# Kernel tuning notes

Hardware: AMD Instinct MI355X
Metric: run time of the kernel (lower is better)

The kernel has to match this reference:

```python
import jax, jax.numpy as jnp
import numpy as np

# --- SLAYER params (nmnistNet.yaml) ---
THETA = 10.0
TS = 1.0
TAU_REF = 1.0
SCALE_REF = 2.0
T_SAMPLE = 300
B = 8

def _alpha_kernel(tau, mult, t_sample, ts, eps=0.01):
    vals = []
    t = 0.0
    while t < t_sample:
        v = mult * t / tau * np.exp(1.0 - t / tau)
        if abs(v) < eps and t > tau:
            break
        vals.append(v)
        t += ts
    return np.asarray(vals, np.float32)

# refractory kernel: alpha kernel with mult = -scaleRef*theta (slayer._calculateRefKernel)
REF_KERNEL = _alpha_kernel(TAU_REF, -SCALE_REF * THETA, T_SAMPLE, TS)
NREF = REF_KERNEL.shape[0]  # 11 for these params; REF_KERNEL[0] == 0


def spike(u):
    """slayerCuda.getSpikes: per-neuron sequential threshold recurrence over time.
    u: [..., T] membrane potential. On spike at t, REF_KERNEL is accumulated
    into u[t:t+NREF]; spike amplitude is 1/Ts."""
    uT = jnp.moveaxis(u, -1, 0)  # [T, ...]
    refk = jnp.asarray(REF_KERNEL[1:]).reshape((NREF - 1,) + (1,) * (u.ndim - 1))
    buf0 = jnp.zeros((NREF - 1,) + uT.shape[1:], u.dtype)  # pending refractory

    def step(buf, u_t):
        u_mod = u_t + buf[0]
        ev = (u_mod >= THETA).astype(u.dtype)
        buf = jnp.concatenate([buf[1:], jnp.zeros_like(buf[:1])], axis=0) + ev[None] * refk
        return buf, ev / TS

    _, s = jax.lax.scan(step, buf0, uT)
    return jnp.moveaxis(s, 0, -1)


def conv2d_t(x, w, pad):
    """slayer.conv: Conv3d with kernel (k,k,1) == per-timestep 2D conv.
    x: [B,C,H,W,T], w: [O,I,kh,kw]."""
    b, c, h, wd, t = x.shape
    xb = jnp.moveaxis(x, -1, 1).reshape(b * t, c, h, wd)
    y = jax.lax.conv_general_dilated(xb, w, (1, 1), [(pad, pad), (pad, pad)],
                                     dimension_numbers=('NCHW', 'OIHW', 'NCHW'))
    o, ho, wo = y.shape[1], y.shape[2], y.shape[3]
    return jnp.moveaxis(y.reshape(b, t, o, ho, wo), 1, -1)


def sum_pool2(x):
    """slayer.pool(2): fixed-weight (1.1*theta) 2x2/stride-2 sum over H,W per channel."""
    y = jax.lax.reduce_window(x, 0.0, jax.lax.add, (1, 1, 2, 2, 1), (1, 1, 2, 2, 1), 'VALID')
    return 1.1 * THETA * y


def setup_inputs():
    key = jax.random.key(0)
    k0, k1, k2, k3, k4 = jax.random.split(key, 5)
    spikeInput = (jax.random.uniform(k0, (B, 2, 34, 34, T_SAMPLE)) < 0.1).astype(jnp.float32) / TS
    # conv weights: kaiming-uniform bound * 100 (the __init__ scales conv weights by 100)
    w1 = jax.random.uniform(k1, (16, 2, 5, 5), minval=-14.1, maxval=14.1, dtype=jnp.float32)
    w2 = jax.random.uniform(k2, (32, 16, 3, 3), minval=-8.3, maxval=8.3, dtype=jnp.float32)
    w3 = jax.random.uniform(k3, (64, 32, 3, 3), minval=-5.9, maxval=5.9, dtype=jnp.float32)
    wfc = jax.random.uniform(k4, (10, 64, 8, 8), minval=-0.5, maxval=0.5, dtype=jnp.float32)
    return {"spikeInput": spikeInput, "w1": w1, "w2": w2, "w3": w3, "wfc": wfc}


def reference(spikeInput, w1, w2, w3, wfc):
    s1 = spike(conv2d_t(spikeInput, w1, 1))  # [B,16,32,32,T]
    s2 = spike(sum_pool2(s1))                # [B,16,16,16,T]
    s3 = spike(conv2d_t(s2, w2, 1))          # [B,32,16,16,T]
    s4 = spike(sum_pool2(s3))                # [B,32,8,8,T]
    s5 = spike(conv2d_t(s4, w3, 1))          # [B,64,8,8,T]
    # dense((8,8,64),10): Conv3d(64,10,(8,8,1)) == full-spatial contraction
    u = jnp.einsum('bchwt,ochw->bot', s5, wfc)[:, :, None, None, :]
    return spike(u)                          # [B,10,1,1,T]
```

## Files before the change

### kernel.cpp

```cpp
#include <hip/hip_runtime.h>
#include <hip/hip_bf16.h>
#include <cmath>

#define T_SAMPLE 300
#define NCHUNK 75

typedef __attribute__((ext_vector_type(8))) short short8;
typedef __attribute__((ext_vector_type(4))) float f32x4;

struct RefK { float v[10]; };

__device__ __forceinline__ unsigned char spike_step(float u, float* buf, const RefK& rk) {
    const float um = u + buf[0];
    const bool fire = um >= 10.0f;
    const float ev = fire ? 1.0f : 0.0f;
#pragma unroll
    for (int r = 0; r < 9; ++r) buf[r] = fmaf(ev, rk.v[r], buf[r + 1]);
    buf[9] = ev * rk.v[9];
    return fire ? (unsigned char)1 : (unsigned char)0;
}

__device__ __forceinline__ short8 bytes_to_bf16x8(uint2 w8) {
    union { uint4 u; short8 s8; } cv;
    cv.u.x = (w8.x & 0xFFu) * 0x3F80u | ((((w8.x >> 8) & 0xFFu) * 0x3F80u) << 16);
    cv.u.y = ((w8.x >> 16) & 0xFFu) * 0x3F80u | ((((w8.x >> 24) & 0xFFu) * 0x3F80u) << 16);
    cv.u.z = (w8.y & 0xFFu) * 0x3F80u | ((((w8.y >> 8) & 0xFFu) * 0x3F80u) << 16);
    cv.u.w = ((w8.y >> 16) & 0xFFu) * 0x3F80u | ((((w8.y >> 24) & 0xFFu) * 0x3F80u) << 16);
    return cv.s8;
}

__device__ __forceinline__ unsigned short bf16_split_sel(float w, int s) {
    __hip_bfloat16 hb = __float2bfloat16(w);
    const float hf = __bfloat162float(hb);
    __hip_bfloat16 mb = __float2bfloat16(w - hf);
    const float mf = __bfloat162float(mb);
    __hip_bfloat16 lb = __float2bfloat16(w - hf - mf);
    __hip_bfloat16 sel = (s == 0) ? hb : ((s == 1) ? mb : lb);
    return *(unsigned short*)&sel;
}

__global__ __launch_bounds__(256) void transpose_in_k(
    const float* __restrict__ In, unsigned int* __restrict__ X)
{
    __shared__ unsigned int lds[16 * NCHUNK];
    const int blk = blockIdx.x;
    const int tn = threadIdx.x >> 4;
    const int tq = threadIdx.x & 15;
    const size_t n = (size_t)blk * 16 + tn;
#pragma unroll
    for (int p = 0; p < 5; ++p) {
        const int ch = p * 16 + tq;
        if (ch < NCHUNK) {
            const float4 v = *(const float4*)(In + n * T_SAMPLE + ch * 4);
            unsigned int u = (v.x != 0.f ? 1u : 0u) | (v.y != 0.f ? 0x100u : 0u) |
                             (v.z != 0.f ? 0x10000u : 0u) | (v.w != 0.f ? 0x1000000u : 0u);
            lds[tn * NCHUNK + ch] = u;
        }
    }
    __syncthreads();
    for (int idx = threadIdx.x; idx < 16 * NCHUNK; idx += 256) {
        const int ch = idx >> 4, t2 = idx & 15;
        X[(size_t)ch * 18496 + blk * 16 + t2] = lds[t2 * NCHUNK + ch];
    }
}

__global__ __launch_bounds__(256) void prep_w1_k(
    const float* __restrict__ w1, unsigned short* __restrict__ Wr1)
{
    const int g = blockIdx.x * 256 + threadIdx.x;
    const int j = g & 7;
    const int lane = (g >> 3) & 63;
    const int ks = (g >> 9) & 3;
    const int s = g >> 11;
    const int q = lane >> 4;
    const int oc = lane & 15;
    const int kg = ks * 32 + q * 8 + j;
    const int slot = kg >> 2, c = kg & 1;
    const int dy = slot / 6, dx = slot % 6;
    const float w = (dy < 5 && dx < 5) ? w1[((oc * 2 + c) * 5 + dy) * 5 + dx] * 0.5f : 0.f;
    Wr1[g] = bf16_split_sel(w, s);
}

__global__ __launch_bounds__(256) void prep_w3_k(
    const float* __restrict__ w3, unsigned short* __restrict__ Wr)
{
    const int g = blockIdx.x * 256 + threadIdx.x;
    const int j = g & 7;
    const int lane = (g >> 3) & 63;
    const int mt = (g >> 9) & 3;
    const int rest = g >> 11;
    const int ks = rest % 9;
    const int s = rest / 9;
    const int oc = mt * 16 + (lane & 15);
    const int ic = (lane >> 4) * 8 + j;
    Wr[g] = bf16_split_sel(w3[(oc * 32 + ic) * 9 + ks], s);
}

__global__ __launch_bounds__(256) void prep_w2_k(
    const float* __restrict__ w2, unsigned short* __restrict__ Wr2)
{
    const int g = blockIdx.x * 256 + threadIdx.x;
    const int j = g & 7;
    const int lane = (g >> 3) & 63;
    const int mt = (g >> 9) & 1;
    const int rest = g >> 10;
    const int kp = rest % 5;
    const int s = rest / 5;
    const int q = lane >> 4;
    const int oc = mt * 16 + (lane & 15);
    const int tap = kp * 2 + (q >> 1);
    const int ic = (q & 1) * 8 + j;
    const float w = (tap <= 8) ? w2[(oc * 16 + ic) * 9 + tap] : 0.f;
    Wr2[g] = bf16_split_sel(w, s);
}

__global__ __launch_bounds__(64) void conv1sp_k(
    const unsigned int* __restrict__ X, const unsigned short* __restrict__ Wr1,
    uchar4* __restrict__ S1, RefK rk)
{
    __shared__ unsigned int tab[25 * 4 * 72];
    const int pg = blockIdx.x;
    const int b = blockIdx.y;
    const int ty = pg >> 2, tx = pg & 3;
    const int lane = threadIdx.x;
    const int q = lane >> 4, n = lane & 15;
    const int py0 = n >> 3, px0 = n & 7;

    short8 Af[12];
#pragma unroll
    for (int s = 0; s < 3; ++s)
#pragma unroll
        for (int ks = 0; ks < 4; ++ks)
            Af[s * 4 + ks] = *(const short8*)(Wr1 + (((s * 4 + ks) * 64 + lane) * 8));

    int offA[4], offB[4];
#pragma unroll
    for (int ks = 0; ks < 4; ++ks) {
        const int sA = ks * 8 + q * 2, sB = sA + 1;
        const int dyA = sA / 6, dxA = sA - dyA * 6;
        const int dyB = sB / 6, dxB = sB - dyB * 6;
        offA[ks] = min(py0 + dyA, 5) * 12 + min(px0 + dxA, 11);
        offB[ks] = min(py0 + dyB, 5) * 12 + min(px0 + dxB, 11);
    }

    int lidx[29];
    int gof[29];
#pragma unroll
    for (int i = 0; i < 29; ++i) {
        const int e = i * 64 + lane;
        if (e < 1800) {
            const int chl = e / 72, site = e - chl * 72;
            const int r = site / 12, cc = site - r * 12;
            const int gy = ty * 2 - 1 + r, gx = tx * 8 - 1 + cc;
            lidx[i] = chl * 288 + site;
            gof[i] = (((unsigned)gy < 34u) && ((unsigned)gx < 34u))
                   ? (chl * 18496 + (b * 2) * 1156 + gy * 34 + gx) : -1;
        } else { lidx[i] = -1; gof[i] = -1; }
    }

    unsigned int w0[29], w1[29];
#pragma unroll
    for (int i = 0; i < 29; ++i) {
        if (gof[i] >= 0) { w0[i] = X[gof[i]]; w1[i] = X[gof[i] + 1156]; }
        else { w0[i] = 0u; w1[i] = 0u; }
    }

    float buf[4][10];
#pragma unroll
    for (int rr = 0; rr < 4; ++rr)
#pragma unroll
        for (int r = 0; r < 10; ++r) buf[rr][r] = 0.f;

    const int nb0 = (b * 16 + q * 4) * 1024 + (ty * 2 + py0) * 32 + tx * 8 + px0;

    for (int st = 0; st < 3; ++st) {
#pragma unroll
        for (int i = 0; i < 29; ++i) {
            if (lidx[i] >= 0) {
#pragma unroll
                for (int t = 0; t < 4; ++t)
                    tab[lidx[i] + t * 72] =
                        ((w0[i] >> (8 * t)) & 0xFFu) * 0x3F80u
                        | ((((w1[i] >> (8 * t)) & 0xFFu) * 0x3F80u) << 16);
            }
        }
        __syncthreads();

        if (st < 2) {
            const unsigned int* Xs = X + (size_t)(st + 1) * (25 * 18496);
#pragma unroll
            for (int i = 0; i < 29; ++i) {
                if (gof[i] >= 0) { w0[i] = Xs[gof[i]]; w1[i] = Xs[gof[i] + 1156]; }
            }
        }

        for (int chl = 0; chl < 25; ++chl) {
            const int ch = st * 25 + chl;
            const unsigned int* tb = tab + chl * 288;

            f32x4 acc[4];
#pragma unroll
            for (int t = 0; t < 4; ++t) acc[t] = (f32x4){0.f, 0.f, 0.f, 0.f};

#pragma unroll
            for (int ks = 0; ks < 4; ++ks)
#pragma unroll
                for (int t = 0; t < 4; ++t) {
                    const unsigned int vA = tb[t * 72 + offA[ks]];
                    const unsigned int vB = tb[t * 72 + offB[ks]];
                    union { uint4 u; short8 s8; } cv;
                    cv.u.x = vA; cv.u.y = vA; cv.u.z = vB; cv.u.w = vB;
#pragma unroll
                    for (int s = 0; s < 3; ++s)
                        acc[t] = __builtin_amdgcn_mfma_f32_16x16x32_bf16(
                            Af[s * 4 + ks], cv.s8, acc[t], 0, 0, 0);
                }

#pragma unroll
            for (int rr = 0; rr < 4; ++rr) {
                uchar4 o;
                o.x = spike_step(acc[0][rr], buf[rr], rk);
                o.y = spike_step(acc[1][rr], buf[rr], rk);
                o.z = spike_step(acc[2][rr], buf[rr], rk);
                o.w = spike_step(acc[3][rr], buf[rr], rk);
                S1[(size_t)ch * 131072 + nb0 + rr * 1024] = o;
            }
        }
        __syncthreads();
    }
}

__global__ __launch_bounds__(256) void conv2_mfma_k(
    const unsigned int* __restrict__ s2u, const unsigned short* __restrict__ Wr2,
    float4* __restrict__ U, int b0, int nbl)
{
    __shared__ __align__(16) unsigned char pad[4 * 18 * 18 * 16];
    const int tc = blockIdx.x;
    const int bl = blockIdx.z;
    const int b = b0 + bl;
    const int tid = threadIdx.x;
    const int wv = tid >> 6, lane = tid & 63;
    const int q = lane >> 4, n = lane & 15;
    const int PLANE_U = nbl * 8192;

    unsigned int* lp = (unsigned int*)pad;
    for (int i = tid; i < 5184; i += 256) lp[i] = 0u;
    __syncthreads();
    const unsigned int* sb = s2u + (size_t)tc * 32768 + b * 4096;
    for (int e = tid; e < 4096; e += 256) {
        const unsigned int v = sb[e];
        const int c = e >> 8, pix = e & 255;
        const int base = (((pix >> 4) + 1) * 18 + ((pix & 15) + 1)) * 16 + c;
        pad[base]         = (unsigned char)(v & 0xFFu);
        pad[5184 + base]  = (unsigned char)((v >> 8) & 0xFFu);
        pad[10368 + base] = (unsigned char)((v >> 16) & 0xFFu);
        pad[15552 + base] = (unsigned char)(v >> 24);
    }
    __syncthreads();

    for (int i = 0; i < 4; ++i) {
        const int r = wv * 4 + i;
        f32x4 acc[2][4];
#pragma unroll
        for (int mt = 0; mt < 2; ++mt)
#pragma unroll
            for (int t = 0; t < 4; ++t) acc[mt][t] = (f32x4){0.f, 0.f, 0.f, 0.f};

        for (int kp = 0; kp < 5; ++kp) {
            short8 Af[6];
#pragma unroll
            for (int s = 0; s < 3; ++s)
#pragma unroll
                for (int mt = 0; mt < 2; ++mt)
                    Af[s * 2 + mt] = *(const short8*)(Wr2 + ((((s * 5 + kp) * 2 + mt) * 64 + lane) * 8));
            int tap = kp * 2 + (q >> 1);
            if (tap > 8) tap = 8;
            const int dy = tap / 3, dx = tap % 3;
#pragma unroll
            for (int t = 0; t < 4; ++t) {
                const int off = ((t * 18 + r + dy) * 18 + (n + dx)) * 16 + (q & 1) * 8;
                const short8 Bf = bytes_to_bf16x8(*(const uint2*)(pad + off));
#pragma unroll
                for (int s = 0; s < 3; ++s)
#pragma unroll
                    for (int mt = 0; mt < 2; ++mt)
                        acc[mt][t] = __builtin_amdgcn_mfma_f32_16x16x32_bf16(
                            Af[s * 2 + mt], Bf, acc[mt][t], 0, 0, 0);
            }
        }

        const size_t ub = (size_t)tc * PLANE_U;
#pragma unroll
        for (int mt = 0; mt < 2; ++mt)
#pragma unroll
            for (int rr = 0; rr < 4; ++rr) {
                const int oc = mt * 16 + q * 4 + rr;
                const int nb = (bl * 32 + oc) * 256 + r * 16 + n;
                U[ub + nb] = make_float4(acc[mt][0][rr], acc[mt][1][rr], acc[mt][2][rr], acc[mt][3][rr]);
            }
    }
}

__global__ __launch_bounds__(256) void conv3_mfma_k(
    const unsigned int* __restrict__ s4u, const unsigned short* __restrict__ Wr,
    float4* __restrict__ U)
{
    __shared__ __align__(16) unsigned char pad[12800];
    const int tc = blockIdx.x;
    const int bl = blockIdx.z;
    const int tid = threadIdx.x;
    const int wv = tid >> 6, lane = tid & 63;
    const int q = lane >> 4, n = lane & 15;

    unsigned int* lp = (unsigned int*)pad;
    for (int i = tid; i < 3200; i += 256) lp[i] = 0u;
    __syncthreads();
    const unsigned int* sb = s4u + (size_t)tc * 16384 + bl * 2048;
    for (int e = tid; e < 2048; e += 256) {
        const unsigned int v = sb[e];
        const int c = e >> 6, pix = e & 63;
        const int base = (((pix >> 3) + 1) * 10 + ((pix & 7) + 1)) * 32 + c;
        pad[base]        = (unsigned char)(v & 0xFFu);
        pad[3200 + base] = (unsigned char)((v >> 8) & 0xFFu);
        pad[6400 + base] = (unsigned char)((v >> 16) & 0xFFu);
        pad[9600 + base] = (unsigned char)(v >> 24);
    }
    __syncthreads();

    const int pixel = wv * 16 + n;
    const int py0 = pixel >> 3, px0 = pixel & 7;

    f32x4 acc[4][4];
#pragma unroll
    for (int mt = 0; mt < 4; ++mt)
#pragma unroll
        for (int t = 0; t < 4; ++t) acc[mt][t] = (f32x4){0.f, 0.f, 0.f, 0.f};

    for (int ks = 0; ks < 9; ++ks) {
        const int dy = ks / 3, dx = ks % 3;
        short8 Af[12];
#pragma unroll
        for (int s = 0; s < 3; ++s)
#pragma unroll
            for (int mt = 0; mt < 4; ++mt)
                Af[s * 4 + mt] = *(const short8*)(Wr + ((((s * 9 + ks) * 4 + mt) * 64 + lane) * 8));
#pragma unroll
        for (int t = 0; t < 4; ++t) {
            const int off = ((t * 10 + py0 + dy) * 10 + (px0 + dx)) * 32 + q * 8;
            const short8 Bf = bytes_to_bf16x8(*(const uint2*)(pad + off));
#pragma unroll
            for (int s = 0; s < 3; ++s)
#pragma unroll
                for (int mt = 0; mt < 4; ++mt)
                    acc[mt][t] = __builtin_amdgcn_mfma_f32_16x16x32_bf16(
                        Af[s * 4 + mt], Bf, acc[mt][t], 0, 0, 0);
        }
    }

    const size_t ub = (size_t)tc * 32768 + (size_t)bl * 4096;
#pragma unroll
    for (int mt = 0; mt < 4; ++mt)
#pragma unroll
        for (int r = 0; r < 4; ++r) {
            const int oc = mt * 16 + q * 4 + r;
            const int nb = oc * 64 + wv * 16 + n;
            U[ub + nb] = make_float4(acc[mt][0][r], acc[mt][1][r], acc[mt][2][r], acc[mt][3][r]);
        }
}

__device__ __forceinline__ void spike_body(
    const float4* __restrict__ U, uchar4* __restrict__ S,
    int nneur, int sstride, int soff, const RefK& rk)
{
    const int n = blockIdx.x * 64 + threadIdx.x;
    const float4* up = U + n;
    uchar4* sp = S + soff + n;
    float buf[10];
#pragma unroll
    for (int r = 0; r < 10; ++r) buf[r] = 0.f;

    float4 ring[8];
#pragma unroll
    for (int r = 0; r < 8; ++r) ring[r] = up[(size_t)r * nneur];

#pragma unroll 8
    for (int ch = 0; ch < 72; ++ch) {
        const float4 cur = ring[ch & 7];
        const int pf = (ch + 8 < NCHUNK) ? ch + 8 : NCHUNK - 1;
        ring[ch & 7] = up[(size_t)pf * nneur];
        uchar4 o;
        o.x = spike_step(cur.x, buf, rk);
        o.y = spike_step(cur.y, buf, rk);
        o.z = spike_step(cur.z, buf, rk);
        o.w = spike_step(cur.w, buf, rk);
        sp[(size_t)ch * sstride] = o;
    }
#pragma unroll
    for (int ch = 72; ch < NCHUNK; ++ch) {
        const float4 cur = ring[ch & 7];
        uchar4 o;
        o.x = spike_step(cur.x, buf, rk);
        o.y = spike_step(cur.y, buf, rk);
        o.z = spike_step(cur.z, buf, rk);
        o.w = spike_step(cur.w, buf, rk);
        sp[(size_t)ch * sstride] = o;
    }
}

__global__ __launch_bounds__(64) void spike2_k(
    const float4* U, uchar4* S, int nneur, int sstride, int soff, RefK rk)
{ spike_body(U, S, nneur, sstride, soff, rk); }

__global__ __launch_bounds__(64) void spike3_k(
    const float4* U, uchar4* S, int nneur, int sstride, int soff, RefK rk)
{ spike_body(U, S, nneur, sstride, soff, rk); }

__device__ __forceinline__ int bsum4(uint2 r0, uint2 r1, int k) {
    return (int)((r0.x >> (8 * k)) & 0xffu) + (int)((r0.y >> (8 * k)) & 0xffu)
         + (int)((r1.x >> (8 * k)) & 0xffu) + (int)((r1.y >> (8 * k)) & 0xffu);
}

template <int C, int H, int W>
__device__ __forceinline__ void pool_body(
    const uchar4* __restrict__ Sin, uchar4* __restrict__ Sout, const RefK& rk)
{
    constexpr int H2 = H / 2, W2 = W / 2;
    constexpr int SIN = 8 * C * H * W;
    constexpr int SOUT = 8 * C * H2 * W2;
    const int n = blockIdx.x * 64 + threadIdx.x;
    const int x = n % W2;
    const int y = (n / W2) % H2;
    const int c = (n / (W2 * H2)) % C;
    const int b = n / (W2 * H2 * C);
    const int base = (((b * C + c) * H + 2 * y) * W + 2 * x);
    uchar4* q = Sout + n;

    float buf[10];
#pragma unroll
    for (int r = 0; r < 10; ++r) buf[r] = 0.f;

    uint2 r0[8], r1[8];
#pragma unroll
    for (int r = 0; r < 8; ++r) {
        r0[r] = *(const uint2*)(Sin + (size_t)r * SIN + base);
        r1[r] = *(const uint2*)(Sin + (size_t)r * SIN + base + W);
    }

#pragma unroll 8
    for (int ch = 0; ch < 72; ++ch) {
        const uint2 a0 = r0[ch & 7], a1 = r1[ch & 7];
        const int pf = (ch + 8 < NCHUNK) ? ch + 8 : NCHUNK - 1;
        r0[ch & 7] = *(const uint2*)(Sin + (size_t)pf * SIN + base);
        r1[ch & 7] = *(const uint2*)(Sin + (size_t)pf * SIN + base + W);
        uchar4 o;
        o.x = spike_step(11.0f * (float)bsum4(a0, a1, 0), buf, rk);
        o.y = spike_step(11.0f * (float)bsum4(a0, a1, 1), buf, rk);
        o.z = spike_step(11.0f * (float)bsum4(a0, a1, 2), buf, rk);
        o.w = spike_step(11.0f * (float)bsum4(a0, a1, 3), buf, rk);
        q[(size_t)ch * SOUT] = o;
    }
#pragma unroll
    for (int ch = 72; ch < NCHUNK; ++ch) {
        const uint2 a0 = r0[ch & 7], a1 = r1[ch & 7];
        uchar4 o;
        o.x = spike_step(11.0f * (float)bsum4(a0, a1, 0), buf, rk);
        o.y = spike_step(11.0f * (float)bsum4(a0, a1, 1), buf, rk);
        o.z = spike_step(11.0f * (float)bsum4(a0, a1, 2), buf, rk);
        o.w = spike_step(11.0f * (float)bsum4(a0, a1, 3), buf, rk);
        q[(size_t)ch * SOUT] = o;
    }
}

__global__ __launch_bounds__(64) void pool2_k(
    const uchar4* Sin, uchar4* Sout, RefK rk) { pool_body<16, 32, 32>(Sin, Sout, rk); }
__global__ __launch_bounds__(64) void pool4_k(
    const uchar4* Sin, uchar4* Sout, RefK rk) { pool_body<32, 16, 16>(Sin, Sout, rk); }

__global__ __launch_bounds__(64) void dense_k(
    const uchar4* __restrict__ S5, const float* __restrict__ WFC,
    float4* __restrict__ U6)
{
    const int tc = blockIdx.x, o = blockIdx.y, b = blockIdx.z;
    const int lane = threadIdx.x;
    float a0 = 0.f, a1 = 0.f, a2 = 0.f, a3 = 0.f;
    const uchar4* sb = S5 + (size_t)tc * 32768 + b * 4096;
    const float* wb = WFC + o * 4096;
    for (int i = 0; i < 64; ++i) {
        const int site = i * 64 + lane;
        const uchar4 s = sb[site];
        const float w = wb[site];
        a0 = fmaf(w, (float)s.x, a0);
        a1 = fmaf(w, (float)s.y, a1);
        a2 = fmaf(w, (float)s.z, a2);
        a3 = fmaf(w, (float)s.w, a3);
    }
#pragma unroll
    for (int m = 1; m < 64; m <<= 1) {
        a0 += __shfl_xor(a0, m, 64);
        a1 += __shfl_xor(a1, m, 64);
        a2 += __shfl_xor(a2, m, 64);
        a3 += __shfl_xor(a3, m, 64);
    }
    if (lane == 0)
        U6[(size_t)tc * 80 + b * 10 + o] = make_float4(a0, a1, a2, a3);
}

__global__ __launch_bounds__(128) void spike6_k(
    const float4* __restrict__ U6, float* __restrict__ Out, RefK rk)
{
    const int n = threadIdx.x;
    if (n >= 80) return;
    const float4* up = U6 + n;
    float* op = Out + (size_t)n * T_SAMPLE;
    float buf[10];
#pragma unroll
    for (int r = 0; r < 10; ++r) buf[r] = 0.f;

    float4 ring[8];
#pragma unroll
    for (int r = 0; r < 8; ++r) ring[r] = up[(size_t)r * 80];

#pragma unroll 8
    for (int ch = 0; ch < 72; ++ch) {
        const float4 cur = ring[ch & 7];
        const int pf = (ch + 8 < NCHUNK) ? ch + 8 : NCHUNK - 1;
        ring[ch & 7] = up[(size_t)pf * 80];
        float4 o;
        o.x = (float)spike_step(cur.x, buf, rk);
        o.y = (float)spike_step(cur.y, buf, rk);
        o.z = (float)spike_step(cur.z, buf, rk);
        o.w = (float)spike_step(cur.w, buf, rk);
        *(float4*)(op + ch * 4) = o;
    }
#pragma unroll
    for (int ch = 72; ch < NCHUNK; ++ch) {
        const float4 cur = ring[ch & 7];
        float4 o;
        o.x = (float)spike_step(cur.x, buf, rk);
        o.y = (float)spike_step(cur.y, buf, rk);
        o.z = (float)spike_step(cur.z, buf, rk);
        o.w = (float)spike_step(cur.w, buf, rk);
        *(float4*)(op + ch * 4) = o;
    }
}

extern "C" void kernel_launch(void* const* d_in, const int* in_sizes, int n_in,
                              void* d_out, int out_size, void* d_ws, size_t ws_size,
                              hipStream_t stream)
{
    const float* spikeIn = (const float*)d_in[0];
    const float* w1 = (const float*)d_in[1];
    const float* w2 = (const float*)d_in[2];
    const float* w3 = (const float*)d_in[3];
    const float* wfc = (const float*)d_in[4];
    float* out = (float*)d_out;

    RefK rk;
    for (int t = 1; t <= 10; ++t)
        rk.v[t - 1] = (float)(-20.0 * (double)t * std::exp(1.0 - (double)t));

    const size_t A_BYTES = 39321600;
    const size_t B_BYTES = 9830400;
    const size_t U6_BYTES = 96000;
    const size_t U_BIG = 78643200, U_SMALL = 39321600;
    const size_t TAIL = A_BYTES + B_BYTES + U6_BYTES;
    const bool big = ws_size >= U_BIG + TAIL;
    const size_t U_BYTES = big ? U_BIG : U_SMALL;

    char* ws = (char*)d_ws;
    float4* U = (float4*)ws;
    uchar4* A = (uchar4*)(ws + U_BYTES);
    uchar4* Bb = (uchar4*)(ws + U_BYTES + A_BYTES);
    float4* U6 = (float4*)(ws + U_BYTES + A_BYTES + B_BYTES);
    unsigned short* Wr = (unsigned short*)(ws + U_BYTES + 20971520);
    unsigned short* Wr2 = (unsigned short*)(ws + U_BYTES + 20971520 + 131072);
    unsigned short* Wr1 = (unsigned short*)(ws + U_BYTES + A_BYTES + 5570560);

    uchar4* X = Bb;
    uchar4* s1 = A;
    uchar4* s2 = Bb;
    uchar4* s3 = A;
    uchar4* s4 = Bb;
    uchar4* s5 = A;

    transpose_in_k<<<18496 / 16, 256, 0, stream>>>(spikeIn, (unsigned int*)X);
    prep_w1_k<<<24, 256, 0, stream>>>(w1, Wr1);

    {
        dim3 g1(64, 8);
        conv1sp_k<<<g1, 64, 0, stream>>>((const unsigned int*)X, Wr1, s1, rk);
    }
    pool2_k<<<32768 / 64, 64, 0, stream>>>(s1, s2, rk);
    prep_w2_k<<<60, 256, 0, stream>>>(w2, Wr2);
    prep_w3_k<<<216, 256, 0, stream>>>(w3, Wr);
    const int nbl2 = big ? 8 : 4;
    for (int b0 = 0; b0 < 8; b0 += nbl2) {
        dim3 g2(NCHUNK, 1, nbl2);
        conv2_mfma_k<<<g2, 256, 0, stream>>>((const unsigned int*)s2, Wr2, U, b0, nbl2);
        const int nn = nbl2 * 8192;
        spike2_k<<<nn / 64, 64, 0, stream>>>(U, s3, nn, 65536, b0 * 8192, rk);
    }
    pool4_k<<<16384 / 64, 64, 0, stream>>>(s3, s4, rk);
    {
        dim3 g3(NCHUNK, 1, 8);
        conv3_mfma_k<<<g3, 256, 0, stream>>>((const unsigned int*)s4, Wr, U);
        spike3_k<<<32768 / 64, 64, 0, stream>>>(U, s5, 32768, 32768, 0, rk);
    }
    dim3 g6(NCHUNK, 10, 8);
    dense_k<<<g6, 64, 0, stream>>>(s5, wfc, U6);
    spike6_k<<<1, 128, 0, stream>>>(U6, out, rk);
}
```

Measured before the change: 296.1 us.

## Vectorize conv1 LDS table layout and software-pipeline MFMA with spike recurrence

Changes the shared-memory table in the conv1+spike kernel to interleave the four timesteps per site, so writes and reads become single 128-bit LDS accesses instead of four scalar ones. Also double-buffers the accumulators so the MFMA chunk for the next channel is issued before the serial spike recurrence of the previous one, letting matrix work overlap the scalar dependency chain. This costs extra accumulator registers, which may raise register pressure in a 64-thread block.

```diff
diff --git a/kernel.cpp b/kernel.cpp
--- a/kernel.cpp
+++ b/kernel.cpp
@@ -114,11 +114,49 @@
     Wr2[g] = bf16_split_sel(w, s);
 }
 
+__device__ __forceinline__ void c1_mfma_chunk(
+    const unsigned int* __restrict__ tb, const int* offA, const int* offB,
+    const short8* Af, f32x4* acc)
+{
+#pragma unroll
+    for (int t = 0; t < 4; ++t) acc[t] = (f32x4){0.f, 0.f, 0.f, 0.f};
+#pragma unroll
+    for (int ks = 0; ks < 4; ++ks) {
+        union { uint4 v; unsigned int u[4]; } va, vb;
+        va.v = *(const uint4*)(tb + offA[ks] * 4);
+        vb.v = *(const uint4*)(tb + offB[ks] * 4);
+#pragma unroll
+        for (int t = 0; t < 4; ++t) {
+            union { uint4 u; short8 s8; } cv;
+            cv.u.x = va.u[t]; cv.u.y = va.u[t]; cv.u.z = vb.u[t]; cv.u.w = vb.u[t];
+#pragma unroll
+            for (int s = 0; s < 3; ++s)
+                acc[t] = __builtin_amdgcn_mfma_f32_16x16x32_bf16(
+                    Af[s * 4 + ks], cv.s8, acc[t], 0, 0, 0);
+        }
+    }
+}
+
+__device__ __forceinline__ void c1_spike_store(
+    const f32x4* acc, float (*buf)[10], const RefK& rk,
+    uchar4* __restrict__ S1, int ch, int nb0)
+{
+#pragma unroll
+    for (int rr = 0; rr < 4; ++rr) {
+        uchar4 o;
+        o.x = spike_step(acc[0][rr], buf[rr], rk);
+        o.y = spike_step(acc[1][rr], buf[rr], rk);
+        o.z = spike_step(acc[2][rr], buf[rr], rk);
+        o.w = spike_step(acc[3][rr], buf[rr], rk);
+        S1[(size_t)ch * 131072 + nb0 + rr * 1024] = o;
+    }
+}
+
 __global__ __launch_bounds__(64) void conv1sp_k(
     const unsigned int* __restrict__ X, const unsigned short* __restrict__ Wr1,
     uchar4* __restrict__ S1, RefK rk)
 {
-    __shared__ unsigned int tab[25 * 4 * 72];
+    __shared__ __align__(16) unsigned int tab[25 * 72 * 4];
     const int pg = blockIdx.x;
     const int b = blockIdx.y;
     const int ty = pg >> 2, tx = pg & 3;
@@ -143,7 +181,7 @@
         offB[ks] = min(py0 + dyB, 5) * 12 + min(px0 + dxB, 11);
     }
 
-    int lidx[29];
+    int lidx4[29];
     int gof[29];
 #pragma unroll
     for (int i = 0; i < 29; ++i) {
@@ -152,10 +190,10 @@
             const int chl = e / 72, site = e - chl * 72;
             const int r = site / 12, cc = site - r * 12;
             const int gy = ty * 2 - 1 + r, gx = tx * 8 - 1 + cc;
-            lidx[i] = chl * 288 + site;
+            lidx4[i] = (chl * 72 + site) * 4;
             gof[i] = (((unsigned)gy < 34u) && ((unsigned)gx < 34u))
                    ? (chl * 18496 + (b * 2) * 1156 + gy * 34 + gx) : -1;
-        } else { lidx[i] = -1; gof[i] = -1; }
+        } else { lidx4[i] = -1; gof[i] = -1; }
     }
 
     unsigned int w0[29], w1[29];
@@ -173,15 +211,18 @@
 
     const int nb0 = (b * 16 + q * 4) * 1024 + (ty * 2 + py0) * 32 + tx * 8 + px0;
 
+    f32x4 accA[4], accB[4];
+
     for (int st = 0; st < 3; ++st) {
 #pragma unroll
         for (int i = 0; i < 29; ++i) {
-            if (lidx[i] >= 0) {
-#pragma unroll
-                for (int t = 0; t < 4; ++t)
-                    tab[lidx[i] + t * 72] =
-                        ((w0[i] >> (8 * t)) & 0xFFu) * 0x3F80u
-                        | ((((w1[i] >> (8 * t)) & 0xFFu) * 0x3F80u) << 16);
+            if (lidx4[i] >= 0) {
+                uint4 val;
+                val.x = (w0[i] & 0xFFu) * 0x3F80u | (((w1[i] & 0xFFu) * 0x3F80u) << 16);
+                val.y = ((w0[i] >> 8) & 0xFFu) * 0x3F80u | ((((w1[i] >> 8) & 0xFFu) * 0x3F80u) << 16);
+                val.z = ((w0[i] >> 16) & 0xFFu) * 0x3F80u | ((((w1[i] >> 16) & 0xFFu) * 0x3F80u) << 16);
+                val.w = ((w0[i] >> 24) & 0xFFu) * 0x3F80u | ((((w1[i] >> 24) & 0xFFu) * 0x3F80u) << 16);
+                *(uint4*)(tab + lidx4[i]) = val;
             }
         }
         __syncthreads();
@@ -194,38 +235,15 @@
             }
         }
 
-        for (int chl = 0; chl < 25; ++chl) {
-            const int ch = st * 25 + chl;
-            const unsigned int* tb = tab + chl * 288;
-
-            f32x4 acc[4];
-#pragma unroll
-            for (int t = 0; t < 4; ++t) acc[t] = (f32x4){0.f, 0.f, 0.f, 0.f};
-
-#pragma unroll
-            for (int ks = 0; ks < 4; ++ks)
-#pragma unroll
-                for (int t = 0; t < 4; ++t) {
-                    const unsigned int vA = tb[t * 72 + offA[ks]];
-                    const unsigned int vB = tb[t * 72 + offB[ks]];
-                    union { uint4 u; short8 s8; } cv;
-                    cv.u.x = vA; cv.u.y = vA; cv.u.z = vB; cv.u.w = vB;
-#pragma unroll
-                    for (int s = 0; s < 3; ++s)
-                        acc[t] = __builtin_amdgcn_mfma_f32_16x16x32_bf16(
-                            Af[s * 4 + ks], cv.s8, acc[t], 0, 0, 0);
-                }
-
-#pragma unroll
-            for (int rr = 0; rr < 4; ++rr) {
-                uchar4 o;
-                o.x = spike_step(acc[0][rr], buf[rr], rk);
-                o.y = spike_step(acc[1][rr], buf[rr], rk);
-                o.z = spike_step(acc[2][rr], buf[rr], rk);
-                o.w = spike_step(acc[3][rr], buf[rr], rk);
-                S1[(size_t)ch * 131072 + nb0 + rr * 1024] = o;
-            }
-        }
+        const int ch0 = st * 25;
+        c1_mfma_chunk(tab, offA, offB, Af, accA);
+        for (int pp = 0; pp < 12; ++pp) {
+            c1_mfma_chunk(tab + (2 * pp + 1) * 288, offA, offB, Af, accB);
+            c1_spike_store(accA, buf, rk, S1, ch0 + 2 * pp, nb0);
+            c1_mfma_chunk(tab + (2 * pp + 2) * 288, offA, offB, Af, accA);
+            c1_spike_store(accB, buf, rk, S1, ch0 + 2 * pp + 1, nb0);
+        }
+        c1_spike_store(accA, buf, rk, S1, ch0 + 24, nb0);
         __syncthreads();
     }
 }
```

New measurement: 296.6 us. About the same (+0.2%).
